# Performance work log

Hardware: AMD Instinct MI355X
Metric: run time of the kernel (lower is better)

Reference implementation:

```python
import jax, jax.numpy as jnp
import numpy as np

N, E, FDIM, H = 50000, 1_600_000, 256, 128


def setup_inputs() -> dict:
    key = jax.random.key(0)
    ks = jax.random.split(key, 16)
    s = 0.05
    return {
        "node_features": jax.random.normal(ks[0], (N, FDIM), dtype=jnp.float32),
        "edge_index": jax.random.randint(ks[1], (2, E), 0, N, dtype=jnp.int64),
        # node encoder: Linear(F,H) -> ReLU -> Linear(H,H)
        "enc_w1": jax.random.normal(ks[2], (FDIM, H), dtype=jnp.float32) * s,
        "enc_b1": jnp.zeros((H,), dtype=jnp.float32),
        "enc_w2": jax.random.normal(ks[3], (H, H), dtype=jnp.float32) * s,
        "enc_b2": jnp.zeros((H,), dtype=jnp.float32),
        # three GCNConv layers (weight + bias each)
        "conv_w1": jax.random.normal(ks[4], (H, H), dtype=jnp.float32) * s,
        "conv_b1": jnp.zeros((H,), dtype=jnp.float32),
        "conv_w2": jax.random.normal(ks[5], (H, H), dtype=jnp.float32) * s,
        "conv_b2": jnp.zeros((H,), dtype=jnp.float32),
        "conv_w3": jax.random.normal(ks[6], (H, H), dtype=jnp.float32) * s,
        "conv_b3": jnp.zeros((H,), dtype=jnp.float32),
        # edge classifier: Linear(2H,H) -> ReLU -> Dropout(eval: identity) -> Linear(H,1) -> Sigmoid
        "cls_w1": jax.random.normal(ks[7], (2 * H, H), dtype=jnp.float32) * s,
        "cls_b1": jnp.zeros((H,), dtype=jnp.float32),
        "cls_w2": jax.random.normal(ks[8], (H, 1), dtype=jnp.float32) * s,
        "cls_b2": jnp.zeros((1,), dtype=jnp.float32),
    }


def _gcn_conv(x, w, b, src, dst, norm, n):
    # GCNConv: x' = scatter_add_dst(norm * (x W)[src]) + b  (self-loops already in src/dst/norm)
    xw = x @ w
    out = jax.ops.segment_sum(xw[src] * norm[:, None], dst, num_segments=n)
    return out + b


def reference(node_features, edge_index, enc_w1, enc_b1, enc_w2, enc_b2,
              conv_w1, conv_b1, conv_w2, conv_b2, conv_w3, conv_b3,
              cls_w1, cls_b1, cls_w2, cls_b2):
    n = node_features.shape[0]
    loops = jnp.arange(n, dtype=edge_index.dtype)
    src = jnp.concatenate([edge_index[0], loops])  # (E+N,)
    dst = jnp.concatenate([edge_index[1], loops])
    # symmetric normalization with self-loops (PyG gcn_norm defaults)
    deg = jax.ops.segment_sum(jnp.ones(src.shape, node_features.dtype), dst, num_segments=n)
    dis = jnp.where(deg > 0, jax.lax.rsqrt(jnp.maximum(deg, 1.0)), 0.0)
    norm = dis[src] * dis[dst]  # (E+N,)

    # node encoder
    x = jax.nn.relu(node_features @ enc_w1 + enc_b1) @ enc_w2 + enc_b2
    # stacked GCN layers
    x = jax.nn.relu(_gcn_conv(x, conv_w1, conv_b1, src, dst, norm, n))
    x = jax.nn.relu(_gcn_conv(x, conv_w2, conv_b2, src, dst, norm, n))
    x = _gcn_conv(x, conv_w3, conv_b3, src, dst, norm, n)

    # edge features: gather + concat  -> (E, 2H)
    ef = jnp.concatenate([x[edge_index[0]], x[edge_index[1]]], axis=1)
    h = jax.nn.relu(ef @ cls_w1 + cls_b1)  # Dropout is identity at eval
    scores = jax.nn.sigmoid(h @ cls_w2 + cls_b2)
    return scores.squeeze(-1)  # (E,)
```

## Files before the change

### kernel.cpp

```cpp
#include <hip/hip_runtime.h>
#include <math.h>

#define HDIM 128
#define BSH 7
#define MAXBUCK 512

typedef __attribute__((ext_vector_type(8))) short    bf16x8;
typedef __attribute__((ext_vector_type(4))) float    f32x4;
typedef __attribute__((ext_vector_type(2))) float    f32x2;
typedef __attribute__((ext_vector_type(8))) unsigned short u16x8;
typedef __attribute__((ext_vector_type(4))) unsigned short u16x4;
typedef __attribute__((ext_vector_type(2))) __fp16 f16x2;

__device__ __forceinline__ float bf2f(unsigned short u) {
    union { unsigned int i; float f; } c; c.i = ((unsigned int)u) << 16; return c.f;
}
__device__ __forceinline__ unsigned short f2bf(float f) {
    union { float f; unsigned int i; } c; c.f = f;
    unsigned int r = (c.i + 0x7fffu + ((c.i >> 16) & 1u)) >> 16;
    return (unsigned short)r;
}
__device__ __forceinline__ void f8x8_decp(uint2 v, f32x2* p) {
    p[0] = __builtin_amdgcn_cvt_pk_f32_fp8((int)v.x, false);
    p[1] = __builtin_amdgcn_cvt_pk_f32_fp8((int)v.x, true);
    p[2] = __builtin_amdgcn_cvt_pk_f32_fp8((int)v.y, false);
    p[3] = __builtin_amdgcn_cvt_pk_f32_fp8((int)v.y, true);
}
__device__ __forceinline__ void f8x16_dech(uint4 v, f16x2* h) {
    f32x2 p[8];
    p[0] = __builtin_amdgcn_cvt_pk_f32_fp8((int)v.x, false);
    p[1] = __builtin_amdgcn_cvt_pk_f32_fp8((int)v.x, true);
    p[2] = __builtin_amdgcn_cvt_pk_f32_fp8((int)v.y, false);
    p[3] = __builtin_amdgcn_cvt_pk_f32_fp8((int)v.y, true);
    p[4] = __builtin_amdgcn_cvt_pk_f32_fp8((int)v.z, false);
    p[5] = __builtin_amdgcn_cvt_pk_f32_fp8((int)v.z, true);
    p[6] = __builtin_amdgcn_cvt_pk_f32_fp8((int)v.w, false);
    p[7] = __builtin_amdgcn_cvt_pk_f32_fp8((int)v.w, true);
#pragma unroll
    for (int i = 0; i < 8; i++) h[i] = __builtin_amdgcn_cvt_pkrtz(p[i].x, p[i].y);
}
__device__ __forceinline__ f16x2 pkmax0(f16x2 a) {
    f16x2 r;
    asm("v_pk_max_f16 %0, %1, 0" : "=v"(r) : "v"(a));
    return r;
}
__device__ __forceinline__ float edot16(uint4 pv, const f16x2 (&qh)[8], const f16x2 (&wh)[8]) {
    f16x2 ph[8]; f8x16_dech(pv, ph);
    float acc = 0.f;
#pragma unroll
    for (int i = 0; i < 8; i++)
        acc = __builtin_amdgcn_fdot2(pkmax0(ph[i] + qh[i]), wh[i], acc, false);
    return acc;
}
__device__ __forceinline__ float fsigmoid(float x) {
    float e = __builtin_amdgcn_exp2f(-x * 1.44269504f);
    return __builtin_amdgcn_rcpf(1.f + e);
}

__global__ __launch_bounds__(256) void k_hist(
    const int* __restrict__ dst, int* __restrict__ tot,
    int* __restrict__ hist, int E, int chunk, int nbuck)
{
    __shared__ int h[MAXBUCK];
    for (int i = threadIdx.x; i < MAXBUCK; i += 256) h[i] = 0;
    __syncthreads();
    int beg = blockIdx.x * chunk;
    int fin = min(beg + chunk, E);
    for (int e = beg + threadIdx.x; e < fin; e += 256)
        atomicAdd(&h[dst[e] >> BSH], 1);
    __syncthreads();
    for (int k = threadIdx.x; k < nbuck; k += 256) {
        int v = h[k];
        hist[(size_t)blockIdx.x * nbuck + k] = v;
        if (v) atomicAdd(&tot[k], v);
    }
}

__global__ __launch_bounds__(256) void k_scan_buckets(
    const int* __restrict__ tot, int* __restrict__ gcur, int* __restrict__ base, int nbuck,
    const float* __restrict__ w2src, unsigned short* __restrict__ w2h)
{
    __shared__ int a[MAXBUCK], b[MAXBUCK];
    int t = threadIdx.x;
    if (t < 128) w2h[t] = __builtin_bit_cast(unsigned short, (__fp16)w2src[t]);
    for (int i = t; i < MAXBUCK; i += 256) a[i] = (i < nbuck) ? tot[i] : 0;
    __syncthreads();
    int* s1 = a; int* s2 = b;
    for (int off = 1; off < MAXBUCK; off <<= 1) {
        for (int i = t; i < MAXBUCK; i += 256)
            s2[i] = s1[i] + ((i >= off) ? s1[i - off] : 0);
        __syncthreads();
        int* tmp = s1; s1 = s2; s2 = tmp;
    }
    for (int i = t; i < nbuck; i += 256) {
        int e = (i == 0) ? 0 : s1[i - 1];
        gcur[i] = e;
        base[i] = e;
    }
    if (t == 0) base[nbuck] = s1[nbuck - 1];
}

__global__ __launch_bounds__(256) void k_partition(
    const int* __restrict__ src, const int* __restrict__ dst,
    const int* __restrict__ hist, int* __restrict__ gcur,
    uint2* __restrict__ stag, int E, int chunk, int nbuck)
{
    __shared__ int h[MAXBUCK];
    int t = threadIdx.x;
    for (int k = t; k < nbuck; k += 256) {
        int v = hist[(size_t)blockIdx.x * nbuck + k];
        h[k] = v ? atomicAdd(&gcur[k], v) : 0;
    }
    __syncthreads();
    int beg = blockIdx.x * chunk;
    int fin = min(beg + chunk, E);
    for (int e = beg + t; e < fin; e += 256) {
        unsigned int d = (unsigned int)dst[e];
        unsigned int s = (unsigned int)src[e];
        int pos = atomicAdd(&h[d >> BSH], 1);
        stag[pos] = make_uint2(s | (d << 16), (unsigned int)e);
    }
}

__global__ __launch_bounds__(256) void k_bucket_csr(
    const int* __restrict__ base, const uint2* __restrict__ stag,
    int* __restrict__ row_ptr, int* __restrict__ col, uint2* __restrict__ epk,
    float* __restrict__ dis, int n, int nbuck)
{
    __shared__ int cl[128], sa[128], sb[128], cur[128];
    int k = blockIdx.x;
    int n0 = k << BSH;
    int t = threadIdx.x;
    if (t < 128) cl[t] = 0;
    __syncthreads();
    int b0 = base[k];
    int m = base[k + 1] - b0;
    const uint2* seg = stag + b0;
    for (int i = t; i < m; i += 256) atomicAdd(&cl[(seg[i].x >> 16) & 127], 1);
    __syncthreads();
    int cv = 0;
    if (t < 128) { cv = cl[t]; sa[t] = cv; }
    __syncthreads();
    int* s1 = sa; int* s2 = sb;
    for (int off = 1; off < 128; off <<= 1) {
        if (t < 128) s2[t] = s1[t] + ((t >= off) ? s1[t - off] : 0);
        __syncthreads();
        int* tmp = s1; s1 = s2; s2 = tmp;
    }
    if (t < 128) {
        int node = n0 + t;
        if (node < n) {
            int rpv = b0 + s1[t] - cv;
            row_ptr[node] = rpv;
            cur[t] = rpv;
            dis[node] = rsqrtf(1.0f + (float)cv);
        }
    }
    if (k == 0 && t == 0) row_ptr[n] = base[nbuck];
    __syncthreads();
    for (int i = t; i < m; i += 256) {
        uint2 e = seg[i];
        int pos = atomicAdd(&cur[(e.x >> 16) & 127], 1);
        int s = (int)(e.x & 0xffffu);
        col[pos] = s;
        epk[pos] = make_uint2((unsigned int)s, e.y);
    }
}

struct WEnt { const float* src; unsigned short* dst; int K; };
struct WAll { WEnt w[7]; };

__global__ __launch_bounds__(256) void k_prep_w(WAll all) {
    WEnt e = all.w[blockIdx.y];
    int i = blockIdx.x * 256 + threadIdx.x;
    if (i >= e.K * HDIM) return;
    int k = i >> 7, c = i & 127;
    e.dst[(size_t)c * e.K + k] = f2bf(e.src[i]);
}

__global__ __launch_bounds__(256) void k_gemm_b(
    const unsigned short* __restrict__ X, const unsigned short* __restrict__ Wt,
    const float* __restrict__ bias, const float* __restrict__ scale,
    void* __restrict__ C, int M, int relu_out, int out_mode)
{
    __shared__ unsigned short sW[128 * 128];
    const int t = threadIdx.x;
#pragma unroll
    for (int i = 0; i < 8; i++) {
        int c = t + i * 256;
        int row = c >> 4, o = c & 15;
        int mt = row >> 4, r = row & 15, kc = o >> 2, q = o & 3;
        int lidx = (mt * 4 + kc) * 64 + q * 16 + r;
        *(uint4*)(sW + (size_t)lidx * 8) = *(const uint4*)(Wt + (size_t)c * 8);
    }
    __syncthreads();
    int wave = t >> 6, lane = t & 63;
    int quad = lane >> 4, r = lane & 15;
    int row0 = blockIdx.x * 64 + wave * 16;
    if (row0 >= M) return;
    const unsigned short* xp = X + (size_t)(row0 + r) * 128 + quad * 8;
    f32x4 acc[8];
#pragma unroll
    for (int mt = 0; mt < 8; mt++) acc[mt] = (f32x4){0.f, 0.f, 0.f, 0.f};
#pragma unroll
    for (int kc = 0; kc < 4; kc++) {
        bf16x8 xf = *(const bf16x8*)(xp + kc * 32);
#pragma unroll
        for (int mt = 0; mt < 8; mt++) {
            bf16x8 wf = *(const bf16x8*)(sW + ((size_t)((mt * 4 + kc) * 64 + lane)) * 8);
            acc[mt] = __builtin_amdgcn_mfma_f32_16x16x32_bf16(wf, xf, acc[mt], 0, 0, 0);
        }
    }
    float sc = scale ? scale[row0 + r] : 1.f;
    if (out_mode == 1) {
        unsigned char* cp = (unsigned char*)C + (size_t)(row0 + r) * HDIM + quad * 4;
#pragma unroll
        for (int mt = 0; mt < 8; mt++) {
            float v[4];
#pragma unroll
            for (int j = 0; j < 4; j++) {
                float x = acc[mt][j];
                if (bias) x += bias[mt * 16 + quad * 4 + j];
                if (relu_out) x = fmaxf(x, 0.f);
                v[j] = x * sc;
            }
            int wd = 0;
            wd = __builtin_amdgcn_cvt_pk_fp8_f32(v[0], v[1], wd, false);
            wd = __builtin_amdgcn_cvt_pk_fp8_f32(v[2], v[3], wd, true);
            *(unsigned int*)(cp + mt * 16) = (unsigned int)wd;
        }
    } else {
        unsigned short* cp = (unsigned short*)C + (size_t)(row0 + r) * HDIM + quad * 4;
#pragma unroll
        for (int mt = 0; mt < 8; mt++) {
            u16x4 o;
#pragma unroll
            for (int j = 0; j < 4; j++) {
                float v = acc[mt][j];
                if (bias) v += bias[mt * 16 + quad * 4 + j];
                if (relu_out) v = fmaxf(v, 0.f);
                o[j] = f2bf(v * sc);
            }
            *(u16x4*)(cp + mt * 16) = o;
        }
    }
}

__global__ __launch_bounds__(256) void k_gemm_nf(
    const float* __restrict__ X, const unsigned short* __restrict__ Wt,
    const float* __restrict__ bias, unsigned short* __restrict__ C,
    int M, int relu_out)
{
    const int K = 256;
    __shared__ unsigned short sW[128 * 256];
    const int t = threadIdx.x;
#pragma unroll
    for (int i = 0; i < 16; i++) {
        int c = t + i * 256;
        int row = c >> 5, o = c & 31;
        int mt = row >> 4, r = row & 15, kc = o >> 2, q = o & 3;
        int lidx = (mt * 8 + kc) * 64 + q * 16 + r;
        *(uint4*)(sW + (size_t)lidx * 8) = *(const uint4*)(Wt + (size_t)c * 8);
    }
    __syncthreads();
    int wave = t >> 6, lane = t & 63;
    int quad = lane >> 4, r = lane & 15;
    int row0 = blockIdx.x * 64 + wave * 16;
    if (row0 >= M) return;
    const float* xp = X + (size_t)(row0 + r) * K + quad * 8;
    f32x4 acc[8];
#pragma unroll
    for (int mt = 0; mt < 8; mt++) acc[mt] = (f32x4){0.f, 0.f, 0.f, 0.f};
#pragma unroll 2
    for (int kc = 0; kc < 8; kc++) {
        float4 xa = *(const float4*)(xp + kc * 32);
        float4 xb = *(const float4*)(xp + kc * 32 + 4);
        bf16x8 xf;
        xf[0] = (short)f2bf(xa.x); xf[1] = (short)f2bf(xa.y);
        xf[2] = (short)f2bf(xa.z); xf[3] = (short)f2bf(xa.w);
        xf[4] = (short)f2bf(xb.x); xf[5] = (short)f2bf(xb.y);
        xf[6] = (short)f2bf(xb.z); xf[7] = (short)f2bf(xb.w);
#pragma unroll
        for (int mt = 0; mt < 8; mt++) {
            bf16x8 wf = *(const bf16x8*)(sW + ((size_t)((mt * 8 + kc) * 64 + lane)) * 8);
            acc[mt] = __builtin_amdgcn_mfma_f32_16x16x32_bf16(wf, xf, acc[mt], 0, 0, 0);
        }
    }
    unsigned short* cp = C + (size_t)(row0 + r) * HDIM + quad * 4;
#pragma unroll
    for (int mt = 0; mt < 8; mt++) {
        u16x4 o;
#pragma unroll
        for (int j = 0; j < 4; j++) {
            float v = acc[mt][j];
            if (bias) v += bias[mt * 16 + quad * 4 + j];
            if (relu_out) v = fmaxf(v, 0.f);
            o[j] = f2bf(v);
        }
        *(u16x4*)(cp + mt * 16) = o;
    }
}

__global__ __launch_bounds__(256) void k_aggregate_f8(
    const int* __restrict__ row_ptr, const int* __restrict__ col,
    const float* __restrict__ dis, const uint2* __restrict__ y8,
    const float* __restrict__ bias, unsigned short* __restrict__ out, int n, int relu_out)
{
    int wid = (blockIdx.x * 256 + threadIdx.x) >> 6;
    if (wid >= n) return;
    int lane = threadIdx.x & 63;
    int q = lane >> 4, t = lane & 15;
    f32x2 acc[4];
    {
        uint2 sv = y8[(size_t)wid * 16 + t];
        f32x2 p[4]; f8x8_decp(sv, p);
#pragma unroll
        for (int i = 0; i < 4; i++) acc[i] = (q == 0) ? p[i] : (f32x2){0.f, 0.f};
    }
    int beg = row_ptr[wid], end = row_ptr[wid + 1];
    int j = beg + q;
    for (; j + 28 < end; j += 32) {
        int s[8];
        uint2 v[8];
#pragma unroll
        for (int u = 0; u < 8; u++) s[u] = col[j + u * 4];
#pragma unroll
        for (int u = 0; u < 8; u++) v[u] = y8[(size_t)s[u] * 16 + t];
#pragma unroll
        for (int u = 0; u < 8; u++) {
            f32x2 p[4]; f8x8_decp(v[u], p);
#pragma unroll
            for (int i = 0; i < 4; i++) acc[i] += p[i];
        }
    }
    for (; j + 12 < end; j += 16) {
        int s0 = col[j], s1 = col[j + 4], s2 = col[j + 8], s3 = col[j + 12];
        uint2 v0 = y8[(size_t)s0 * 16 + t];
        uint2 v1 = y8[(size_t)s1 * 16 + t];
        uint2 v2 = y8[(size_t)s2 * 16 + t];
        uint2 v3 = y8[(size_t)s3 * 16 + t];
        f32x2 p0[4], p1[4], p2[4], p3[4];
        f8x8_decp(v0, p0); f8x8_decp(v1, p1); f8x8_decp(v2, p2); f8x8_decp(v3, p3);
#pragma unroll
        for (int i = 0; i < 4; i++) acc[i] += (p0[i] + p1[i]) + (p2[i] + p3[i]);
    }
    for (; j < end; j += 4) {
        int s = col[j];
        uint2 v = y8[(size_t)s * 16 + t];
        f32x2 p[4]; f8x8_decp(v, p);
#pragma unroll
        for (int i = 0; i < 4; i++) acc[i] += p[i];
    }
#pragma unroll
    for (int i = 0; i < 4; i++) {
        acc[i].x += __shfl_xor(acc[i].x, 16, 64);
        acc[i].y += __shfl_xor(acc[i].y, 16, 64);
        acc[i].x += __shfl_xor(acc[i].x, 32, 64);
        acc[i].y += __shfl_xor(acc[i].y, 32, 64);
    }
    if (q == 0) {
        float di = dis[wid];
        u16x8 o;
#pragma unroll
        for (int i = 0; i < 4; i++) {
            float v0 = di * acc[i].x + bias[t * 8 + i * 2];
            float v1 = di * acc[i].y + bias[t * 8 + i * 2 + 1];
            if (relu_out) { v0 = fmaxf(v0, 0.f); v1 = fmaxf(v1, 0.f); }
            o[i * 2]     = f2bf(v0);
            o[i * 2 + 1] = f2bf(v1);
        }
        *(u16x8*)(out + (size_t)wid * HDIM + t * 8) = o;
    }
}

__global__ __launch_bounds__(256) void k_edge_score_csr(
    const int* __restrict__ row_ptr, const uint2* __restrict__ epk,
    const uint4* __restrict__ P8, const uint4* __restrict__ Q8,
    const unsigned short* __restrict__ w2h, const float* __restrict__ b2,
    float* __restrict__ out, int n)
{
    int wid = (blockIdx.x * 256 + threadIdx.x) >> 6;
    if (wid >= n) return;
    int lane = threadIdx.x & 63;
    unsigned g = (unsigned)(lane >> 3), t = (unsigned)(lane & 7);
    f16x2 wh[8], qh[8];
    {
        uint4 wv0 = *(const uint4*)(w2h + t * 16);
        uint4 wv1 = *(const uint4*)(w2h + t * 16 + 8);
        wh[0] = __builtin_bit_cast(f16x2, wv0.x);
        wh[1] = __builtin_bit_cast(f16x2, wv0.y);
        wh[2] = __builtin_bit_cast(f16x2, wv0.z);
        wh[3] = __builtin_bit_cast(f16x2, wv0.w);
        wh[4] = __builtin_bit_cast(f16x2, wv1.x);
        wh[5] = __builtin_bit_cast(f16x2, wv1.y);
        wh[6] = __builtin_bit_cast(f16x2, wv1.z);
        wh[7] = __builtin_bit_cast(f16x2, wv1.w);
        uint4 qv = Q8[(unsigned)wid * 8u + t];
        f8x16_dech(qv, qh);
    }
    float bb = b2[0];
    int beg = row_ptr[wid], end = row_ptr[wid + 1];
    int j = beg + (int)g;
    for (; j + 24 < end; j += 32) {
        uint2 e0 = epk[j], e1 = epk[j + 8], e2 = epk[j + 16], e3 = epk[j + 24];
        uint4 p0 = P8[e0.x * 8u + t];
        uint4 p1 = P8[e1.x * 8u + t];
        uint4 p2 = P8[e2.x * 8u + t];
        uint4 p3 = P8[e3.x * 8u + t];
        float s0 = edot16(p0, qh, wh);
        float s1 = edot16(p1, qh, wh);
        float s2 = edot16(p2, qh, wh);
        float s3 = edot16(p3, qh, wh);
        s0 += __shfl_xor(s0, 4, 8); s1 += __shfl_xor(s1, 4, 8);
        s2 += __shfl_xor(s2, 4, 8); s3 += __shfl_xor(s3, 4, 8);
        s0 += __shfl_xor(s0, 2, 8); s1 += __shfl_xor(s1, 2, 8);
        s2 += __shfl_xor(s2, 2, 8); s3 += __shfl_xor(s3, 2, 8);
        s0 += __shfl_xor(s0, 1, 8); s1 += __shfl_xor(s1, 1, 8);
        s2 += __shfl_xor(s2, 1, 8); s3 += __shfl_xor(s3, 1, 8);
        if (t < 4) {
            float sv = (t == 0) ? s0 : (t == 1) ? s1 : (t == 2) ? s2 : s3;
            unsigned eid = (t == 0) ? e0.y : (t == 1) ? e1.y : (t == 2) ? e2.y : e3.y;
            __builtin_nontemporal_store(fsigmoid(sv + bb), &out[eid]);
        }
    }
    for (; j + 8 < end; j += 16) {
        uint2 e0 = epk[j], e1 = epk[j + 8];
        uint4 p0 = P8[e0.x * 8u + t];
        uint4 p1 = P8[e1.x * 8u + t];
        float s0 = edot16(p0, qh, wh);
        float s1 = edot16(p1, qh, wh);
        s0 += __shfl_xor(s0, 4, 8); s1 += __shfl_xor(s1, 4, 8);
        s0 += __shfl_xor(s0, 2, 8); s1 += __shfl_xor(s1, 2, 8);
        s0 += __shfl_xor(s0, 1, 8); s1 += __shfl_xor(s1, 1, 8);
        if (t < 2) {
            float sv = (t == 0) ? s0 : s1;
            unsigned eid = (t == 0) ? e0.y : e1.y;
            __builtin_nontemporal_store(fsigmoid(sv + bb), &out[eid]);
        }
    }
    if (j < end) {
        uint2 e0 = epk[j];
        uint4 p0 = P8[e0.x * 8u + t];
        float s0 = edot16(p0, qh, wh);
        s0 += __shfl_xor(s0, 4, 8);
        s0 += __shfl_xor(s0, 2, 8);
        s0 += __shfl_xor(s0, 1, 8);
        if (t == 0)
            __builtin_nontemporal_store(fsigmoid(s0 + bb), &out[e0.y]);
    }
}

extern "C" void kernel_launch(void* const* d_in, const int* in_sizes, int n_in,
                              void* d_out, int out_size, void* d_ws, size_t ws_size,
                              hipStream_t stream) {
    const float* nf   = (const float*)d_in[0];
    const int*   ei   = (const int*)d_in[1];
    const float* ew1  = (const float*)d_in[2];
    const float* eb1  = (const float*)d_in[3];
    const float* ew2  = (const float*)d_in[4];
    const float* eb2  = (const float*)d_in[5];
    const float* cw1  = (const float*)d_in[6];
    const float* cb1  = (const float*)d_in[7];
    const float* cw2  = (const float*)d_in[8];
    const float* cb2  = (const float*)d_in[9];
    const float* cw3  = (const float*)d_in[10];
    const float* cb3  = (const float*)d_in[11];
    const float* clw1 = (const float*)d_in[12];
    const float* clb1 = (const float*)d_in[13];
    const float* clw2 = (const float*)d_in[14];
    const float* clb2 = (const float*)d_in[15];
    float* out = (float*)d_out;

    const int FD = 256;
    const int N = in_sizes[0] / FD;
    const int E = in_sizes[1] / 2;
    const int NBUCK = (N + 127) >> BSH;
    const int PBLK = 256;
    const int chunk = (E + PBLK - 1) / PBLK;

    size_t Np = ((size_t)N + 256) & ~(size_t)255;
    char* w = (char*)d_ws;
    float* dis     = (float*)w;            w += Np * 4;
    int*   tot     = (int*)w;              w += MAXBUCK * 4;
    int*   gcur    = (int*)w;              w += MAXBUCK * 4;
    int*   base    = (int*)w;              w += (MAXBUCK + 4) * 4;
    int*   hist    = (int*)w;              w += (size_t)PBLK * MAXBUCK * 4;
    int*   row_ptr = (int*)w;              w += Np * 4;
    uint2* stag    = (uint2*)w;            w += (size_t)E * 8;
    uint2* epk     = (uint2*)w;            w += (size_t)E * 8;
    int*   col     = (int*)w;              w += (((size_t)E * 4) + 255) & ~(size_t)255;
    unsigned short* bufA = (unsigned short*)w;  w += (size_t)N * HDIM * 2;
    unsigned short* bufB = (unsigned short*)w;  w += (size_t)N * HDIM * 2;
    unsigned short* bufC = (unsigned short*)w;  w += (size_t)N * HDIM * 2;
    unsigned char*  f8X  = (unsigned char*)w;   w += ((size_t)N * HDIM + 255) & ~(size_t)255;
    unsigned char*  f8P  = (unsigned char*)w;   w += ((size_t)N * HDIM + 255) & ~(size_t)255;
    unsigned char*  f8Q  = (unsigned char*)w;   w += ((size_t)N * HDIM + 255) & ~(size_t)255;
    unsigned short* wtE1 = (unsigned short*)w;  w += 256 * HDIM * 2;
    unsigned short* wtE2 = (unsigned short*)w;  w += 128 * HDIM * 2;
    unsigned short* wtC1 = (unsigned short*)w;  w += 128 * HDIM * 2;
    unsigned short* wtC2 = (unsigned short*)w;  w += 128 * HDIM * 2;
    unsigned short* wtC3 = (unsigned short*)w;  w += 128 * HDIM * 2;
    unsigned short* wtT  = (unsigned short*)w;  w += 128 * HDIM * 2;
    unsigned short* wtB  = (unsigned short*)w;  w += 128 * HDIM * 2;
    unsigned short* w2h  = (unsigned short*)w;  w += 256 * 2;

    int gemm_grid = (N + 63) / 64;
    int ag = (N + 3) / 4;

    WAll wa;
    wa.w[0] = { ew1,               wtE1, 256 };
    wa.w[1] = { ew2,               wtE2, 128 };
    wa.w[2] = { cw1,               wtC1, 128 };
    wa.w[3] = { cw2,               wtC2, 128 };
    wa.w[4] = { cw3,               wtC3, 128 };
    wa.w[5] = { clw1,              wtT,  128 };
    wa.w[6] = { clw1 + 128 * HDIM, wtB,  128 };
    k_prep_w<<<dim3(128, 7), 256, 0, stream>>>(wa);

    hipMemsetAsync(tot, 0, MAXBUCK * sizeof(int), stream);
    k_hist<<<PBLK, 256, 0, stream>>>(ei + E, tot, hist, E, chunk, NBUCK);
    k_scan_buckets<<<1, 256, 0, stream>>>(tot, gcur, base, NBUCK, clw2, w2h);
    k_partition<<<PBLK, 256, 0, stream>>>(ei, ei + E, hist, gcur, stag, E, chunk, NBUCK);
    k_bucket_csr<<<NBUCK, 256, 0, stream>>>(base, stag, row_ptr, col, epk, dis, N, NBUCK);

    k_gemm_nf<<<gemm_grid, 256, 0, stream>>>(nf, wtE1, eb1, bufA, N, 1);
    k_gemm_b<<<gemm_grid, 256, 0, stream>>>(bufA, wtE2, eb2, nullptr, bufB, N, 0, 0);

    k_gemm_b<<<gemm_grid, 256, 0, stream>>>(bufB, wtC1, nullptr, dis, f8X, N, 0, 1);
    k_aggregate_f8<<<ag, 256, 0, stream>>>(row_ptr, col, dis, (const uint2*)f8X, cb1, bufC, N, 1);
    k_gemm_b<<<gemm_grid, 256, 0, stream>>>(bufC, wtC2, nullptr, dis, f8X, N, 0, 1);
    k_aggregate_f8<<<ag, 256, 0, stream>>>(row_ptr, col, dis, (const uint2*)f8X, cb2, bufA, N, 1);
    k_gemm_b<<<gemm_grid, 256, 0, stream>>>(bufA, wtC3, nullptr, dis, f8X, N, 0, 1);
    k_aggregate_f8<<<ag, 256, 0, stream>>>(row_ptr, col, dis, (const uint2*)f8X, cb3, bufB, N, 0);

    k_gemm_b<<<gemm_grid, 256, 0, stream>>>(bufB, wtT, clb1, nullptr, f8P, N, 0, 1);
    k_gemm_b<<<gemm_grid, 256, 0, stream>>>(bufB, wtB, nullptr, nullptr, f8Q, N, 0, 1);

    k_edge_score_csr<<<ag, 256, 0, stream>>>(row_ptr, epk, (const uint4*)f8P, (const uint4*)f8Q,
                                             w2h, clb2, out, N);
}
```

Measured before the change: 459.5 us.

## Split GCN aggregation into two half-feature passes for cache locality

The GEMM now writes the fp8 transformed features as two separate 64-column tables. Aggregation runs twice per layer, once per half, with 8 lanes per neighbor and 8 neighbors in flight per wave. The aim is to make each gathered table small enough to stay cache-resident during the random neighbor gathers, at the cost of reading the CSR column array twice and launching extra kernels. Separately, the 4-way unrolled loop in the edge-score kernel is removed, leaving the 2-way loop.

```diff
diff --git a/kernel.cpp b/kernel.cpp
--- a/kernel.cpp
+++ b/kernel.cpp
@@ -181,7 +181,7 @@
 __global__ __launch_bounds__(256) void k_gemm_b(
     const unsigned short* __restrict__ X, const unsigned short* __restrict__ Wt,
     const float* __restrict__ bias, const float* __restrict__ scale,
-    void* __restrict__ C, int M, int relu_out, int out_mode)
+    void* __restrict__ C, void* __restrict__ C2, int M, int relu_out, int out_mode)
 {
     __shared__ unsigned short sW[128 * 128];
     const int t = threadIdx.x;
@@ -213,7 +213,10 @@
     }
     float sc = scale ? scale[row0 + r] : 1.f;
     if (out_mode == 1) {
-        unsigned char* cp = (unsigned char*)C + (size_t)(row0 + r) * HDIM + quad * 4;
+        unsigned char* clo = (unsigned char*)C  + ((C2 ? (size_t)(row0 + r) * 64
+                                                      : (size_t)(row0 + r) * HDIM)) + quad * 4;
+        unsigned char* chi = C2 ? (unsigned char*)C2 + (size_t)(row0 + r) * 64 + quad * 4
+                                : clo + 64;
 #pragma unroll
         for (int mt = 0; mt < 8; mt++) {
             float v[4];
@@ -227,7 +230,8 @@
             int wd = 0;
             wd = __builtin_amdgcn_cvt_pk_fp8_f32(v[0], v[1], wd, false);
             wd = __builtin_amdgcn_cvt_pk_fp8_f32(v[2], v[3], wd, true);
-            *(unsigned int*)(cp + mt * 16) = (unsigned int)wd;
+            unsigned char* cp = (mt < 4) ? clo + mt * 16 : chi + (mt - 4) * 16;
+            *(unsigned int*)cp = (unsigned int)wd;
         }
     } else {
         unsigned short* cp = (unsigned short*)C + (size_t)(row0 + r) * HDIM + quad * 4;
@@ -301,75 +305,74 @@
     }
 }
 
-__global__ __launch_bounds__(256) void k_aggregate_f8(
+__global__ __launch_bounds__(256) void k_aggregate_half(
     const int* __restrict__ row_ptr, const int* __restrict__ col,
-    const float* __restrict__ dis, const uint2* __restrict__ y8,
-    const float* __restrict__ bias, unsigned short* __restrict__ out, int n, int relu_out)
+    const float* __restrict__ dis, const uint2* __restrict__ yh,
+    const float* __restrict__ bias, unsigned short* __restrict__ out,
+    int hoff, int n, int relu_out)
 {
     int wid = (blockIdx.x * 256 + threadIdx.x) >> 6;
     if (wid >= n) return;
     int lane = threadIdx.x & 63;
-    int q = lane >> 4, t = lane & 15;
+    unsigned g = (unsigned)(lane >> 3), t = (unsigned)(lane & 7);
     f32x2 acc[4];
     {
-        uint2 sv = y8[(size_t)wid * 16 + t];
+        uint2 sv = yh[(unsigned)wid * 8u + t];
         f32x2 p[4]; f8x8_decp(sv, p);
 #pragma unroll
-        for (int i = 0; i < 4; i++) acc[i] = (q == 0) ? p[i] : (f32x2){0.f, 0.f};
+        for (int i = 0; i < 4; i++) acc[i] = (g == 0) ? p[i] : (f32x2){0.f, 0.f};
     }
     int beg = row_ptr[wid], end = row_ptr[wid + 1];
-    int j = beg + q;
-    for (; j + 28 < end; j += 32) {
-        int s[8];
-        uint2 v[8];
-#pragma unroll
-        for (int u = 0; u < 8; u++) s[u] = col[j + u * 4];
-#pragma unroll
-        for (int u = 0; u < 8; u++) v[u] = y8[(size_t)s[u] * 16 + t];
-#pragma unroll
-        for (int u = 0; u < 8; u++) {
-            f32x2 p[4]; f8x8_decp(v[u], p);
-#pragma unroll
-            for (int i = 0; i < 4; i++) acc[i] += p[i];
-        }
-    }
-    for (; j + 12 < end; j += 16) {
-        int s0 = col[j], s1 = col[j + 4], s2 = col[j + 8], s3 = col[j + 12];
-        uint2 v0 = y8[(size_t)s0 * 16 + t];
-        uint2 v1 = y8[(size_t)s1 * 16 + t];
-        uint2 v2 = y8[(size_t)s2 * 16 + t];
-        uint2 v3 = y8[(size_t)s3 * 16 + t];
+    int j = beg + (int)g;
+    for (; j + 24 < end; j += 32) {
+        unsigned s0 = (unsigned)col[j],      s1 = (unsigned)col[j + 8];
+        unsigned s2 = (unsigned)col[j + 16], s3 = (unsigned)col[j + 24];
+        uint2 v0 = yh[s0 * 8u + t];
+        uint2 v1 = yh[s1 * 8u + t];
+        uint2 v2 = yh[s2 * 8u + t];
+        uint2 v3 = yh[s3 * 8u + t];
         f32x2 p0[4], p1[4], p2[4], p3[4];
         f8x8_decp(v0, p0); f8x8_decp(v1, p1); f8x8_decp(v2, p2); f8x8_decp(v3, p3);
 #pragma unroll
         for (int i = 0; i < 4; i++) acc[i] += (p0[i] + p1[i]) + (p2[i] + p3[i]);
     }
-    for (; j < end; j += 4) {
-        int s = col[j];
-        uint2 v = y8[(size_t)s * 16 + t];
-        f32x2 p[4]; f8x8_decp(v, p);
-#pragma unroll
-        for (int i = 0; i < 4; i++) acc[i] += p[i];
+    for (; j + 8 < end; j += 16) {
+        unsigned s0 = (unsigned)col[j], s1 = (unsigned)col[j + 8];
+        uint2 v0 = yh[s0 * 8u + t];
+        uint2 v1 = yh[s1 * 8u + t];
+        f32x2 p0[4], p1[4];
+        f8x8_decp(v0, p0); f8x8_decp(v1, p1);
+#pragma unroll
+        for (int i = 0; i < 4; i++) acc[i] += p0[i] + p1[i];
+    }
+    if (j < end) {
+        unsigned s0 = (unsigned)col[j];
+        uint2 v0 = yh[s0 * 8u + t];
+        f32x2 p0[4]; f8x8_decp(v0, p0);
+#pragma unroll
+        for (int i = 0; i < 4; i++) acc[i] += p0[i];
     }
 #pragma unroll
     for (int i = 0; i < 4; i++) {
+        acc[i].x += __shfl_xor(acc[i].x, 8, 64);
+        acc[i].y += __shfl_xor(acc[i].y, 8, 64);
         acc[i].x += __shfl_xor(acc[i].x, 16, 64);
         acc[i].y += __shfl_xor(acc[i].y, 16, 64);
         acc[i].x += __shfl_xor(acc[i].x, 32, 64);
         acc[i].y += __shfl_xor(acc[i].y, 32, 64);
     }
-    if (q == 0) {
+    if (g == 0) {
         float di = dis[wid];
         u16x8 o;
 #pragma unroll
         for (int i = 0; i < 4; i++) {
-            float v0 = di * acc[i].x + bias[t * 8 + i * 2];
-            float v1 = di * acc[i].y + bias[t * 8 + i * 2 + 1];
+            float v0 = di * acc[i].x + bias[hoff + t * 8 + i * 2];
+            float v1 = di * acc[i].y + bias[hoff + t * 8 + i * 2 + 1];
             if (relu_out) { v0 = fmaxf(v0, 0.f); v1 = fmaxf(v1, 0.f); }
             o[i * 2]     = f2bf(v0);
             o[i * 2 + 1] = f2bf(v1);
         }
-        *(u16x8*)(out + (size_t)wid * HDIM + t * 8) = o;
+        *(u16x8*)(out + (size_t)wid * HDIM + hoff + t * 8) = o;
     }
 }
 
@@ -401,28 +404,6 @@
     float bb = b2[0];
     int beg = row_ptr[wid], end = row_ptr[wid + 1];
     int j = beg + (int)g;
-    for (; j + 24 < end; j += 32) {
-        uint2 e0 = epk[j], e1 = epk[j + 8], e2 = epk[j + 16], e3 = epk[j + 24];
-        uint4 p0 = P8[e0.x * 8u + t];
-        uint4 p1 = P8[e1.x * 8u + t];
-        uint4 p2 = P8[e2.x * 8u + t];
-        uint4 p3 = P8[e3.x * 8u + t];
-        float s0 = edot16(p0, qh, wh);
-        float s1 = edot16(p1, qh, wh);
-        float s2 = edot16(p2, qh, wh);
-        float s3 = edot16(p3, qh, wh);
-        s0 += __shfl_xor(s0, 4, 8); s1 += __shfl_xor(s1, 4, 8);
-        s2 += __shfl_xor(s2, 4, 8); s3 += __shfl_xor(s3, 4, 8);
-        s0 += __shfl_xor(s0, 2, 8); s1 += __shfl_xor(s1, 2, 8);
-        s2 += __shfl_xor(s2, 2, 8); s3 += __shfl_xor(s3, 2, 8);
-        s0 += __shfl_xor(s0, 1, 8); s1 += __shfl_xor(s1, 1, 8);
-        s2 += __shfl_xor(s2, 1, 8); s3 += __shfl_xor(s3, 1, 8);
-        if (t < 4) {
-            float sv = (t == 0) ? s0 : (t == 1) ? s1 : (t == 2) ? s2 : s3;
-            unsigned eid = (t == 0) ? e0.y : (t == 1) ? e1.y : (t == 2) ? e2.y : e3.y;
-            __builtin_nontemporal_store(fsigmoid(sv + bb), &out[eid]);
-        }
-    }
     for (; j + 8 < end; j += 16) {
         uint2 e0 = epk[j], e1 = epk[j + 8];
         uint4 p0 = P8[e0.x * 8u + t];
@@ -432,11 +413,10 @@
         s0 += __shfl_xor(s0, 4, 8); s1 += __shfl_xor(s1, 4, 8);
         s0 += __shfl_xor(s0, 2, 8); s1 += __shfl_xor(s1, 2, 8);
         s0 += __shfl_xor(s0, 1, 8); s1 += __shfl_xor(s1, 1, 8);
-        if (t < 2) {
-            float sv = (t == 0) ? s0 : s1;
-            unsigned eid = (t == 0) ? e0.y : e1.y;
+        float sv = (t == 0) ? s0 : s1;
+        unsigned eid = (t == 0) ? e0.y : e1.y;
+        if (t < 2)
             __builtin_nontemporal_store(fsigmoid(sv + bb), &out[eid]);
-        }
     }
     if (j < end) {
         uint2 e0 = epk[j];
@@ -492,7 +472,8 @@
     unsigned short* bufA = (unsigned short*)w;  w += (size_t)N * HDIM * 2;
     unsigned short* bufB = (unsigned short*)w;  w += (size_t)N * HDIM * 2;
     unsigned short* bufC = (unsigned short*)w;  w += (size_t)N * HDIM * 2;
-    unsigned char*  f8X  = (unsigned char*)w;   w += ((size_t)N * HDIM + 255) & ~(size_t)255;
+    unsigned char*  f8Ylo = (unsigned char*)w;  w += ((size_t)N * 64 + 255) & ~(size_t)255;
+    unsigned char*  f8Yhi = (unsigned char*)w;  w += ((size_t)N * 64 + 255) & ~(size_t)255;
     unsigned char*  f8P  = (unsigned char*)w;   w += ((size_t)N * HDIM + 255) & ~(size_t)255;
     unsigned char*  f8Q  = (unsigned char*)w;   w += ((size_t)N * HDIM + 255) & ~(size_t)255;
     unsigned short* wtE1 = (unsigned short*)w;  w += 256 * HDIM * 2;
@@ -524,17 +505,20 @@
     k_bucket_csr<<<NBUCK, 256, 0, stream>>>(base, stag, row_ptr, col, epk, dis, N, NBUCK);
 
     k_gemm_nf<<<gemm_grid, 256, 0, stream>>>(nf, wtE1, eb1, bufA, N, 1);
-    k_gemm_b<<<gemm_grid, 256, 0, stream>>>(bufA, wtE2, eb2, nullptr, bufB, N, 0, 0);
-
-    k_gemm_b<<<gemm_grid, 256, 0, stream>>>(bufB, wtC1, nullptr, dis, f8X, N, 0, 1);
-    k_aggregate_f8<<<ag, 256, 0, stream>>>(row_ptr, col, dis, (const uint2*)f8X, cb1, bufC, N, 1);
-    k_gemm_b<<<gemm_grid, 256, 0, stream>>>(bufC, wtC2, nullptr, dis, f8X, N, 0, 1);
-    k_aggregate_f8<<<ag, 256, 0, stream>>>(row_ptr, col, dis, (const uint2*)f8X, cb2, bufA, N, 1);
-    k_gemm_b<<<gemm_grid, 256, 0, stream>>>(bufA, wtC3, nullptr, dis, f8X, N, 0, 1);
-    k_aggregate_f8<<<ag, 256, 0, stream>>>(row_ptr, col, dis, (const uint2*)f8X, cb3, bufB, N, 0);
-
-    k_gemm_b<<<gemm_grid, 256, 0, stream>>>(bufB, wtT, clb1, nullptr, f8P, N, 0, 1);
-    k_gemm_b<<<gemm_grid, 256, 0, stream>>>(bufB, wtB, nullptr, nullptr, f8Q, N, 0, 1);
+    k_gemm_b<<<gemm_grid, 256, 0, stream>>>(bufA, wtE2, eb2, nullptr, bufB, nullptr, N, 0, 0);
+
+    k_gemm_b<<<gemm_grid, 256, 0, stream>>>(bufB, wtC1, nullptr, dis, f8Ylo, f8Yhi, N, 0, 1);
+    k_aggregate_half<<<ag, 256, 0, stream>>>(row_ptr, col, dis, (const uint2*)f8Ylo, cb1, bufC, 0,  N, 1);
+    k_aggregate_half<<<ag, 256, 0, stream>>>(row_ptr, col, dis, (const uint2*)f8Yhi, cb1, bufC, 64, N, 1);
+    k_gemm_b<<<gemm_grid, 256, 0, stream>>>(bufC, wtC2, nullptr, dis, f8Ylo, f8Yhi, N, 0, 1);
+    k_aggregate_half<<<ag, 256, 0, stream>>>(row_ptr, col, dis, (const uint2*)f8Ylo, cb2, bufA, 0,  N, 1);
+    k_aggregate_half<<<ag, 256, 0, stream>>>(row_ptr, col, dis, (const uint2*)f8Yhi, cb2, bufA, 64, N, 1);
+    k_gemm_b<<<gemm_grid, 256, 0, stream>>>(bufA, wtC3, nullptr, dis, f8Ylo, f8Yhi, N, 0, 1);
+    k_aggregate_half<<<ag, 256, 0, stream>>>(row_ptr, col, dis, (const uint2*)f8Ylo, cb3, bufB, 0,  N, 0);
+    k_aggregate_half<<<ag, 256, 0, stream>>>(row_ptr, col, dis, (const uint2*)f8Yhi, cb3, bufB, 64, N, 0);
+
+    k_gemm_b<<<gemm_grid, 256, 0, stream>>>(bufB, wtT, clb1, nullptr, f8P, nullptr, N, 0, 1);
+    k_gemm_b<<<gemm_grid, 256, 0, stream>>>(bufB, wtB, nullptr, nullptr, f8Q, nullptr, N, 0, 1);
 
     k_edge_score_csr<<<ag, 256, 0, stream>>>(row_ptr, epk, (const uint4*)f8P, (const uint4*)f8Q,
                                              w2h, clb2, out, N);
```

Result: slower. 501.7 us (+9.2%).
